# Kernel tuning notes

Hardware: AMD Instinct MI355X
Metric: run time of the kernel (lower is better)

Reference implementation:

```python
import jax, jax.numpy as jnp
import numpy as np
from jax import lax

N_GROUPS, TOP_K, CALIB_SCALE = 4, 3, 2.0


def setup_inputs() -> dict:
    key = jax.random.key(0)
    ks = jax.random.split(key, 32)
    d = {}
    d['x'] = jax.random.normal(ks[0], (64, 64, 8192), jnp.float32)
    d['conv_weight'] = jax.random.normal(ks[1], (64, 64, 3), jnp.float32) * 0.05
    d['bias'] = jax.random.normal(ks[2], (64,), jnp.float32) * 0.05
    d['grads'] = jax.random.normal(ks[3], (12288,), jnp.float32) * 0.01
    d['q_ema'] = jax.random.normal(ks[4], (4416,), jnp.float32) * 0.1
    d['ctrl_w'] = jax.random.normal(ks[5], (64, 192), jnp.float32) * 0.07
    d['ctrl_b'] = jnp.zeros((64,), jnp.float32)
    d['gp_w'] = jax.random.normal(ks[6], (64, 65), jnp.float32) * 0.1
    d['gp_b'] = jnp.zeros((64,), jnp.float32)
    d['gt_w'] = jax.random.normal(ks[7], (64, 64), jnp.float32) * 0.1
    d['gt_b'] = jnp.zeros((64,), jnp.float32)
    d['ln_g'] = jnp.ones((64,), jnp.float32)
    d['ln_b'] = jnp.zeros((64,), jnp.float32)
    d['ccin_w'] = jax.random.normal(ks[8], (64, 64), jnp.float32) * 0.05
    d['ccin_b'] = jnp.zeros((64,), jnp.float32)
    d['ck_w'] = jax.random.normal(ks[9], (3, 64), jnp.float32) * 0.05
    d['ck_b'] = jnp.zeros((3,), jnp.float32)
    d['cb_w'] = jax.random.normal(ks[10], (1, 64), jnp.float32) * 0.05
    d['cb_b'] = jnp.zeros((1,), jnp.float32)
    d['cf_w'] = jax.random.normal(ks[11], (1, 64), jnp.float32) * 0.05
    d['cf_b'] = jnp.zeros((1,), jnp.float32)
    d['tau_w'] = jax.random.normal(ks[12], (1, 64), jnp.float32) * 0.1
    d['tau_b'] = jnp.zeros((1,), jnp.float32)
    W = jax.random.normal(ks[13], (4, 1104, 32), jnp.float32)
    d['mem_W'] = W / jnp.linalg.norm(W, axis=1, keepdims=True)  # column-normalized codebook
    d['temp_logit'] = jnp.zeros((4,), jnp.float32)
    return d


def reference(x, conv_weight, bias, grads, q_ema, ctrl_w, ctrl_b, gp_w, gp_b,
              gt_w, gt_b, ln_g, ln_b, ccin_w, ccin_b, ck_w, ck_b, cb_w, cb_b,
              cf_w, cf_b, tau_w, tau_b, mem_W, temp_logit):
    C_out, C_in, K = conv_weight.shape
    cpg = C_out // N_GROUPS
    cin_tot, k_tot = C_out * C_in, C_out * K
    shift = 0.0  # shift_magnitude

    # --- controller: grads -> calibration query q ---
    g = grads.reshape(C_out, C_in * K)
    h = jax.nn.silu(g @ ctrl_w.T + ctrl_b)
    gn = jnp.linalg.norm(g, axis=-1, keepdims=True)
    z = jax.nn.sigmoid(jnp.concatenate([h, gn], -1) @ gp_w.T + gp_b)
    h_t = jax.nn.silu(h @ gt_w.T + gt_b)
    hm = (1.0 - z) * h + z * h_t
    mu = hm.mean(-1, keepdims=True)
    var = ((hm - mu) ** 2).mean(-1, keepdims=True)
    h = ln_g * (hm - mu) / jnp.sqrt(var + 1e-5) + ln_b

    w_cin = jnp.tanh(h @ ccin_w.T + ccin_b) * CALIB_SCALE   # [C_out, C_in]
    w_k = jnp.tanh(h @ ck_w.T + ck_b) * CALIB_SCALE         # [C_out, K]
    b_r = jnp.tanh(h @ cb_w.T + cb_b)[:, 0] * CALIB_SCALE   # [C_out]
    f_r = jnp.tanh(h @ cf_w.T + cf_b)[:, 0] * CALIB_SCALE   # [C_out]
    tau = jax.nn.sigmoid(h @ tau_w.T + tau_b).mean() * 0.5 + 0.5

    q = jnp.concatenate([w_cin.reshape(-1), w_k.reshape(-1), b_r, f_r])
    q = 0.7 * q + 0.3 * lax.stop_gradient(q_ema)

    # --- channel-grouped codebook retrieval (trigger path) ---
    qd = lax.stop_gradient(q)
    q_groups = jnp.concatenate([
        qd[:cin_tot].reshape(N_GROUPS, cpg * C_in),
        qd[cin_tot:cin_tot + k_tot].reshape(N_GROUPS, cpg * K),
        qd[cin_tot + k_tot:cin_tot + k_tot + C_out].reshape(N_GROUPS, cpg),
        qd[cin_tot + k_tot + C_out:].reshape(N_GROUPS, cpg)], axis=1)  # [G, gq]
    temp = (jax.nn.sigmoid(temp_logit) * 0.6 + 0.2) / (1.0 + shift)     # [G]
    att = jnp.einsum('gd,gdm->gm', q_groups, mem_W)
    att = jax.nn.softmax(att / (temp[:, None] + 1e-8), axis=1)
    v, idx = lax.top_k(att, TOP_K)                                      # [G, k]
    gath = jnp.take_along_axis(mem_W, idx[:, None, :], axis=2)          # [G, gq, k]
    retrieved = (gath * v[:, None, :]).sum(-1)                          # [G, gq]

    s0, s1, s2 = cpg * C_in, cpg * (C_in + K), cpg * (C_in + K + 1)
    retrieved_global = jnp.concatenate([
        retrieved[:, :s0].reshape(-1),
        retrieved[:, s0:s1].reshape(-1),
        retrieved[:, s1:s2].reshape(-1),
        retrieved[:, s2:].reshape(-1)])
    q = tau * q + (1.0 - tau) * lax.stop_gradient(retrieved_global)

    # --- split q and modulate conv ---
    w_cin = q[:cin_tot].reshape(C_out, C_in)
    w_k = q[cin_tot:cin_tot + k_tot].reshape(C_out, K)
    b_c = q[cin_tot + k_tot:cin_tot + k_tot + C_out]
    f_c = q[cin_tot + k_tot + C_out:]

    w = conv_weight * (1.0 + w_cin)[:, :, None] * (1.0 + w_k)[:, None, :]
    pad = ((K - 1) * 1 + 1) // 2  # receptive_field // 2 (dilation=1)
    out = lax.conv_general_dilated(x, w, window_strides=(1,),
                                   padding=[(pad, pad)], rhs_dilation=(1,),
                                   dimension_numbers=('NCH', 'OIH', 'NCH'))
    out = out + (bias * (1.0 + b_c))[None, :, None]
    out = out * (1.0 + f_c)[None, :, None]
    return out
```

## Files before the change

kernel.cpp:

```cpp
#include <hip/hip_runtime.h>
#include <math.h>

typedef __attribute__((ext_vector_type(8))) short bf16x8;
typedef __attribute__((ext_vector_type(4))) float f32x4;
typedef unsigned long long ull;

__device__ __forceinline__ float sigmoidf_(float x) { return 1.f / (1.f + expf(-x)); }

__device__ __forceinline__ unsigned short f2bf(float f) {
  unsigned int u = __float_as_uint(f);
  u += 0x7fffu + ((u >> 16) & 1u);
  return (unsigned short)(u >> 16);
}

#define WS_BEFF  0
#define WS_SEFF  64
#define WS_WFRAG 128

__global__ __launch_bounds__(1024) void kCtl(
    const float* __restrict__ grads, const float* __restrict__ ctrl_w, const float* __restrict__ ctrl_b,
    const float* __restrict__ gp_w, const float* __restrict__ gp_b,
    const float* __restrict__ gt_w, const float* __restrict__ gt_b,
    const float* __restrict__ ln_g, const float* __restrict__ ln_b,
    const float* __restrict__ ccin_w, const float* __restrict__ ccin_b,
    const float* __restrict__ ck_w, const float* __restrict__ ck_b,
    const float* __restrict__ cb_w, const float* __restrict__ cb_b,
    const float* __restrict__ cf_w, const float* __restrict__ cf_b,
    const float* __restrict__ tau_w, const float* __restrict__ tau_b,
    const float* __restrict__ q_ema, const float* __restrict__ mem_W,
    const float* __restrict__ temp_logit,
    const float* __restrict__ conv_weight, const float* __restrict__ bias,
    float* __restrict__ ws) {
  __shared__ float rawA[8514];
  __shared__ float sh_h[64 * 65];
  __shared__ float gnp[64 * 17];
  __shared__ float taup[64];
  __shared__ float sh_qg[4416];
  __shared__ float part[16][32];
  __shared__ float sv[3];
  __shared__ int sidx[3];
  __shared__ float qc1[16][64];
  __shared__ float qk1[16][3];
  __shared__ float sh_tau;
  const int tid = threadIdx.x;
  const int g = blockIdx.x;
  const int j = tid & 63;
  const int wv = tid >> 6;
  const int i0 = wv * 4;
  const int i0u = __builtin_amdgcn_readfirstlane(i0);

  float acc[4] = {0.f, 0.f, 0.f, 0.f};
  for (int hh = 0; hh < 2; ++hh) {
    const int d0 = hh * 96;
    for (int t = tid; t < 6144; t += 1024) {
      int jj = t / 96, dl = t - jj * 96;
      rawA[dl * 66 + jj] = ctrl_w[jj * 192 + d0 + dl];
    }
    __syncthreads();
    const float* g0 = grads + i0u * 192 + d0;
#pragma unroll 8
    for (int dl = 0; dl < 96; ++dl) {
      float wvv = rawA[dl * 66 + j];
      acc[0] += wvv * g0[dl];
      acc[1] += wvv * g0[192 + dl];
      acc[2] += wvv * g0[384 + dl];
      acc[3] += wvv * g0[576 + dl];
    }
    __syncthreads();
  }
  {
    float cb_ = ctrl_b[j];
#pragma unroll
    for (int ii = 0; ii < 4; ++ii) {
      float s = acc[ii] + cb_;
      sh_h[(i0 + ii) * 65 + j] = s * sigmoidf_(s);
    }
  }
  {
    int gi = tid >> 4, seg = tid & 15;
    const float* gr = grads + gi * 192 + seg * 12;
    float ss = 0.f;
#pragma unroll
    for (int m = 0; m < 12; ++m) { float v = gr[m]; ss += v * v; }
    gnp[gi * 17 + seg] = ss;
  }
  __syncthreads();
  if (tid < 64) {
    float s = 0.f;
#pragma unroll
    for (int seg = 0; seg < 16; ++seg) s += gnp[tid * 17 + seg];
    gnp[tid * 17 + 16] = sqrtf(s);
  }
  for (int t = tid; t < 4096; t += 1024) rawA[(t & 63) * 66 + (t >> 6)] = gt_w[t];
  for (int t = tid; t < 4160; t += 1024) {
    int jj = t / 65, dd = t - jj * 65;
    rawA[4224 + dd * 66 + jj] = gp_w[t];
  }
  __syncthreads();

  float hm[4];
  {
    float zacc[4] = {0.f, 0.f, 0.f, 0.f}, tacc[4] = {0.f, 0.f, 0.f, 0.f};
#pragma unroll 4
    for (int d = 0; d < 64; ++d) {
      float gtv = rawA[d * 66 + j];
      float gpv = rawA[4224 + d * 66 + j];
#pragma unroll
      for (int ii = 0; ii < 4; ++ii) {
        float hv = sh_h[(i0 + ii) * 65 + d];
        tacc[ii] += hv * gtv;
        zacc[ii] += hv * gpv;
      }
    }
    float gplast = rawA[4224 + 64 * 66 + j];
    float zb = gp_b[j], tb = gt_b[j];
#pragma unroll
    for (int ii = 0; ii < 4; ++ii) {
      float gn_ = gnp[(i0 + ii) * 17 + 16];
      float zs = zacc[ii] + gn_ * gplast + zb;
      float ts = tacc[ii] + tb;
      float z = sigmoidf_(zs);
      float ht = ts * sigmoidf_(ts);
      hm[ii] = (1.f - z) * sh_h[(i0 + ii) * 65 + j] + z * ht;
    }
  }
  __syncthreads();
#pragma unroll
  for (int ii = 0; ii < 4; ++ii) sh_h[(i0 + ii) * 65 + j] = hm[ii];
  __syncthreads();

  {
    float lg = ln_g[j], lb = ln_b[j];
#pragma unroll
    for (int ii = 0; ii < 4; ++ii) {
      float x = sh_h[(i0 + ii) * 65 + j];
      float s = x;
#pragma unroll
      for (int off = 32; off; off >>= 1) s += __shfl_xor(s, off);
      float mu = s * (1.f / 64.f);
      float dv = x - mu;
      float v2 = dv * dv;
#pragma unroll
      for (int off = 32; off; off >>= 1) v2 += __shfl_xor(v2, off);
      float invs = 1.f / sqrtf(v2 * (1.f / 64.f) + 1e-5f);
      sh_h[(i0 + ii) * 65 + j] = lg * dv * invs + lb;
    }
  }
  for (int t = tid; t < 4096; t += 1024) rawA[(t & 63) * 66 + (t >> 6)] = ccin_w[t];
  if (tid < 384) {
    int c = tid >> 6, d = tid & 63;
    float v = (c < 3) ? ck_w[c * 64 + d] : (c == 3) ? cb_w[d] : (c == 4) ? cf_w[d] : tau_w[d];
    rawA[4224 + c * 64 + d] = v;
  }
  __syncthreads();

  {
    float cb_ = ccin_b[j];
    float s4[4] = {0.f, 0.f, 0.f, 0.f};
#pragma unroll 4
    for (int d = 0; d < 64; ++d) {
      float cv = rawA[d * 66 + j];
#pragma unroll
      for (int ii = 0; ii < 4; ++ii) s4[ii] += sh_h[(i0 + ii) * 65 + d] * cv;
    }
#pragma unroll
    for (int ii = 0; ii < 4; ++ii) {
      int i = i0 + ii;
      float val = 2.f * tanhf(s4[ii] + cb_);
      sh_qg[(i >> 4) * 1104 + (i & 15) * 64 + j] = 0.7f * val + 0.3f * q_ema[i * 64 + j];
    }
  }
  if (wv < 6) {
    int i = j;
    float s = 0.f;
    const float* er = rawA + 4224 + wv * 64;
#pragma unroll 4
    for (int d = 0; d < 64; ++d) s += sh_h[i * 65 + d] * er[d];
    if (wv < 3) {
      float val = 2.f * tanhf(s + ck_b[wv]);
      sh_qg[(i >> 4) * 1104 + 1024 + (i & 15) * 3 + wv] = 0.7f * val + 0.3f * q_ema[4096 + i * 3 + wv];
    } else if (wv == 3) {
      float val = 2.f * tanhf(s + cb_b[0]);
      sh_qg[(i >> 4) * 1104 + 1072 + (i & 15)] = 0.7f * val + 0.3f * q_ema[4288 + i];
    } else if (wv == 4) {
      float val = 2.f * tanhf(s + cf_b[0]);
      sh_qg[(i >> 4) * 1104 + 1088 + (i & 15)] = 0.7f * val + 0.3f * q_ema[4352 + i];
    } else {
      taup[i] = sigmoidf_(s + tau_b[0]);
    }
  }
  __syncthreads();
  if (tid < 64) {
    float t_ = taup[tid];
#pragma unroll
    for (int off = 32; off; off >>= 1) t_ += __shfl_xor(t_, off);
    if (tid == 0) sh_tau = (t_ * (1.f / 64.f)) * 0.5f + 0.5f;
  }
  __syncthreads();

  const float* mwg = mem_W + (size_t)g * 1104 * 32;
  {
    float4 a = {0.f, 0.f, 0.f, 0.f};
    const float* qg = sh_qg + g * 1104;
#pragma unroll
    for (int it = 0; it < 9; ++it) {
      int d = it * 128 + (tid >> 3);
      if (d < 1104) {
        float4 v4 = *(const float4*)(mwg + (size_t)d * 32 + (tid & 7) * 4);
        float qv = qg[d];
        a.x += qv * v4.x; a.y += qv * v4.y; a.z += qv * v4.z; a.w += qv * v4.w;
      }
    }
#pragma unroll
    for (int off = 8; off <= 32; off <<= 1) {
      a.x += __shfl_xor(a.x, off); a.y += __shfl_xor(a.y, off);
      a.z += __shfl_xor(a.z, off); a.w += __shfl_xor(a.w, off);
    }
    if ((tid & 63) < 8) *(float4*)&part[tid >> 6][(tid & 7) * 4] = a;
  }
  __syncthreads();

  if (tid < 32) {
    int m = tid;
    float att = 0.f;
#pragma unroll
    for (int w = 0; w < 16; ++w) att += part[w][m];
    float temp = 0.6f * sigmoidf_(temp_logit[g]) + 0.2f;
    att /= (temp + 1e-8f);
    float mx = att;
#pragma unroll
    for (int off = 16; off; off >>= 1) mx = fmaxf(mx, __shfl_xor(mx, off, 32));
    float e = expf(att - mx);
    float s = e;
#pragma unroll
    for (int off = 16; off; off >>= 1) s += __shfl_xor(s, off, 32);
    float p = e / s;
    for (int t = 0; t < 3; ++t) {
      float bp = p; int bm = m;
#pragma unroll
      for (int off = 16; off; off >>= 1) {
        float op = __shfl_xor(bp, off, 32);
        int om = __shfl_xor(bm, off, 32);
        if (op > bp || (op == bp && om < bm)) { bp = op; bm = om; }
      }
      if (m == 0) { sv[t] = bp; sidx[t] = bm; }
      if (m == bm) p = -1.f;
    }
  }
  __syncthreads();

  {
    const float tau = sh_tau;
    const float v0 = sv[0], v1 = sv[1], v2 = sv[2];
    const int x0 = sidx[0], x1 = sidx[1], x2 = sidx[2];
    const float* qg = sh_qg + g * 1104;
    int cl = wv;
    int co = 16 * g + cl;
    int lane = j;
    {
      int d = cl * 64 + lane;
      float r = v0 * mwg[(size_t)d * 32 + x0] + v1 * mwg[(size_t)d * 32 + x1] + v2 * mwg[(size_t)d * 32 + x2];
      qc1[cl][lane] = 1.f + tau * qg[d] + (1.f - tau) * r;
    }
    if (lane < 3) {
      int d = 1024 + cl * 3 + lane;
      float r = v0 * mwg[(size_t)d * 32 + x0] + v1 * mwg[(size_t)d * 32 + x1] + v2 * mwg[(size_t)d * 32 + x2];
      qk1[cl][lane] = 1.f + tau * qg[d] + (1.f - tau) * r;
    }
    if (lane == 3) {
      int d = 1072 + cl;
      float r = v0 * mwg[(size_t)d * 32 + x0] + v1 * mwg[(size_t)d * 32 + x1] + v2 * mwg[(size_t)d * 32 + x2];
      float qb = tau * qg[d] + (1.f - tau) * r;
      ws[WS_BEFF + co] = bias[co] * (1.f + qb);
    }
    if (lane == 4) {
      int d = 1088 + cl;
      float r = v0 * mwg[(size_t)d * 32 + x0] + v1 * mwg[(size_t)d * 32 + x1] + v2 * mwg[(size_t)d * 32 + x2];
      ws[WS_SEFF + co] = 1.f + tau * qg[d] + (1.f - tau) * r;
    }
  }
  __syncthreads();

  unsigned short* wfrag = (unsigned short*)(ws + WS_WFRAG);
  for (int idx = tid; idx < 3072; idx += 1024) {
    int cl = idx / 192, rem = idx - cl * 192;
    int kk = rem >> 6, ci = rem & 63;
    int co = 16 * g + cl;
    float val = conv_weight[(co * 64 + ci) * 3 + kk] * qc1[cl][ci] * qk1[cl][kk];
    int e = kk * 64 + ci;
    int s = e >> 5, hi = (e >> 3) & 3, jj = e & 7;
    wfrag[s * 2048 + g * 512 + (16 * hi + cl) * 8 + jj] = f2bf(val);
  }
}

__global__ __launch_bounds__(256, 5) void k3_v7(
    const float* __restrict__ x, const unsigned short* __restrict__ wfrag,
    const float* __restrict__ beff, const float* __restrict__ seff,
    float* __restrict__ out) {
  __shared__ unsigned short xs[130 * 64];
  const int tid = threadIdx.x;
  const int w = tid >> 6, l = tid & 63;
  const int g = l >> 4, c16 = l & 15;
  const int n = blockIdx.y;
  const int l0 = blockIdx.x * 128;

  bf16x8 wf[6];
#pragma unroll
  for (int s = 0; s < 6; ++s)
    wf[s] = *(const bf16x8*)(wfrag + s * 2048 + w * 512 + l * 8);

  {
    const int cp = 8 * w + (l >> 3);
    const float* r0 = x + ((size_t)(n * 64 + 2 * cp)) * 8192 + l0;
    const float* r1 = r0 + 8192;
    char* xb = (char*)xs;
#pragma unroll
    for (int t = 0; t < 4; ++t) {
      int p0 = 4 * ((l & 7) + 8 * t);
      float4 va = *(const float4*)(r0 + p0);
      float4 vb = *(const float4*)(r1 + p0);
      float av[4] = {va.x, va.y, va.z, va.w};
      float bv[4] = {vb.x, vb.y, vb.z, vb.w};
#pragma unroll
      for (int i = 0; i < 4; ++i) {
        int p = p0 + i + 1;
        unsigned u = (unsigned)f2bf(av[i]) | ((unsigned)f2bf(bv[i]) << 16);
        *(unsigned*)(xb + p * 128 + ((4 * cp) ^ ((p & 7) << 4))) = u;
      }
    }
    if ((l & 7) == 0) {
      float a0 = 0.f, b0 = 0.f, a1 = 0.f, b1 = 0.f;
      if (l0 > 0) {
        float4 va = *(const float4*)(r0 - 4);
        float4 vb = *(const float4*)(r1 - 4);
        a0 = va.w; b0 = vb.w;
      }
      if (l0 + 128 < 8192) {
        float4 va = *(const float4*)(r0 + 128);
        float4 vb = *(const float4*)(r1 + 128);
        a1 = va.x; b1 = vb.x;
      }
      unsigned u0 = (unsigned)f2bf(a0) | ((unsigned)f2bf(b0) << 16);
      unsigned u1 = (unsigned)f2bf(a1) | ((unsigned)f2bf(b1) << 16);
      *(unsigned*)(xb + 0 * 128 + (4 * cp)) = u0;
      *(unsigned*)(xb + 129 * 128 + ((4 * cp) ^ 16)) = u1;
    }
  }
  __syncthreads();

  f32x4 acc[8];
#pragma unroll
  for (int t = 0; t < 8; ++t) acc[t] = (f32x4){0.f, 0.f, 0.f, 0.f};

  const char* xbc = (const char*)xs;
#pragma unroll
  for (int s = 0; s < 6; ++s) {
    const int kk = s >> 1;
    const int C = 4 * (s & 1) + g;
#pragma unroll
    for (int nt = 0; nt < 8; ++nt) {
      const int p = 16 * nt + c16 + kk;
      bf16x8 A = *(const bf16x8*)(xbc + p * 128 + ((C ^ (p & 7)) << 4));
      acc[nt] = __builtin_amdgcn_mfma_f32_16x16x32_bf16(A, wf[s], acc[nt], 0, 0, 0);
    }
  }

  const int co = 16 * w + c16;
  const float be = beff[co], se = seff[co];
  float* orow = out + ((size_t)(n * 64 + co)) * 8192 + l0 + 4 * g;
#pragma unroll
  for (int nt = 0; nt < 8; ++nt) {
    float4 ov;
    ov.x = se * (acc[nt][0] + be);
    ov.y = se * (acc[nt][1] + be);
    ov.z = se * (acc[nt][2] + be);
    ov.w = se * (acc[nt][3] + be);
    *(float4*)(orow + nt * 16) = ov;
  }
}

extern "C" void kernel_launch(void* const* d_in, const int* in_sizes, int n_in,
                              void* d_out, int out_size, void* d_ws, size_t ws_size,
                              hipStream_t stream) {
  const float* x = (const float*)d_in[0];
  const float* conv_weight = (const float*)d_in[1];
  const float* bias = (const float*)d_in[2];
  const float* grads = (const float*)d_in[3];
  const float* q_ema = (const float*)d_in[4];
  const float* ctrl_w = (const float*)d_in[5];
  const float* ctrl_b = (const float*)d_in[6];
  const float* gp_w = (const float*)d_in[7];
  const float* gp_b = (const float*)d_in[8];
  const float* gt_w = (const float*)d_in[9];
  const float* gt_b = (const float*)d_in[10];
  const float* ln_g = (const float*)d_in[11];
  const float* ln_b = (const float*)d_in[12];
  const float* ccin_w = (const float*)d_in[13];
  const float* ccin_b = (const float*)d_in[14];
  const float* ck_w = (const float*)d_in[15];
  const float* ck_b = (const float*)d_in[16];
  const float* cb_w = (const float*)d_in[17];
  const float* cb_b = (const float*)d_in[18];
  const float* cf_w = (const float*)d_in[19];
  const float* cf_b = (const float*)d_in[20];
  const float* tau_w = (const float*)d_in[21];
  const float* tau_b = (const float*)d_in[22];
  const float* mem_W = (const float*)d_in[23];
  const float* temp_logit = (const float*)d_in[24];

  float* ws = (float*)d_ws;

  hipLaunchKernelGGL(kCtl, dim3(4), dim3(1024), 0, stream,
                     grads, ctrl_w, ctrl_b, gp_w, gp_b, gt_w, gt_b, ln_g, ln_b,
                     ccin_w, ccin_b, ck_w, ck_b, cb_w, cb_b, cf_w, cf_b,
                     tau_w, tau_b, q_ema, mem_W, temp_logit, conv_weight, bias, ws);
  hipLaunchKernelGGL(k3_v7, dim3(64, 64), dim3(256), 0, stream,
                     x, (const unsigned short*)(ws + WS_WFRAG), ws + WS_BEFF, ws + WS_SEFF,
                     (float*)d_out);
}
```

Baseline: 100.8 us.

## Make conv blocks persistent over four tiles with double-buffered LDS prefetch

Each block now processes four consecutive 128-wide tiles instead of one. Global loads for the next tile are issued before the MFMA work on the current tile and written to the second LDS buffer afterwards. This overlaps the memory traffic with compute and loads the weight fragments once per four tiles. In exchange it launches a quarter as many blocks, uses twice the LDS and holds more live registers, which lowers occupancy (launch bounds drop from 5 to 4).

```diff
diff --git a/kernel.cpp b/kernel.cpp
--- a/kernel.cpp
+++ b/kernel.cpp
@@ -7,10 +7,10 @@
 
 __device__ __forceinline__ float sigmoidf_(float x) { return 1.f / (1.f + expf(-x)); }
 
-__device__ __forceinline__ unsigned short f2bf(float f) {
+__device__ __forceinline__ unsigned f2bf(float f) {
   unsigned int u = __float_as_uint(f);
   u += 0x7fffu + ((u >> 16) & 1u);
-  return (unsigned short)(u >> 16);
+  return u >> 16;
 }
 
 #define WS_BEFF  0
@@ -289,94 +289,124 @@
     float val = conv_weight[(co * 64 + ci) * 3 + kk] * qc1[cl][ci] * qk1[cl][kk];
     int e = kk * 64 + ci;
     int s = e >> 5, hi = (e >> 3) & 3, jj = e & 7;
-    wfrag[s * 2048 + g * 512 + (16 * hi + cl) * 8 + jj] = f2bf(val);
+    wfrag[s * 2048 + g * 512 + (16 * hi + cl) * 8 + jj] = (unsigned short)f2bf(val);
   }
 }
 
-__global__ __launch_bounds__(256, 5) void k3_v7(
+#define TC 4
+__global__ __launch_bounds__(256, 4) void k3_p(
     const float* __restrict__ x, const unsigned short* __restrict__ wfrag,
     const float* __restrict__ beff, const float* __restrict__ seff,
     float* __restrict__ out) {
-  __shared__ unsigned short xs[130 * 64];
+  __shared__ unsigned short xs[2][130 * 64];
   const int tid = threadIdx.x;
   const int w = tid >> 6, l = tid & 63;
   const int g = l >> 4, c16 = l & 15;
   const int n = blockIdx.y;
-  const int l0 = blockIdx.x * 128;
+  const int base = blockIdx.x * (TC * 128);
 
   bf16x8 wf[6];
 #pragma unroll
   for (int s = 0; s < 6; ++s)
     wf[s] = *(const bf16x8*)(wfrag + s * 2048 + w * 512 + l * 8);
 
-  {
-    const int cp = 8 * w + (l >> 3);
-    const float* r0 = x + ((size_t)(n * 64 + 2 * cp)) * 8192 + l0;
-    const float* r1 = r0 + 8192;
-    char* xb = (char*)xs;
-#pragma unroll
-    for (int t = 0; t < 4; ++t) {
-      int p0 = 4 * ((l & 7) + 8 * t);
-      float4 va = *(const float4*)(r0 + p0);
-      float4 vb = *(const float4*)(r1 + p0);
-      float av[4] = {va.x, va.y, va.z, va.w};
-      float bv[4] = {vb.x, vb.y, vb.z, vb.w};
-#pragma unroll
-      for (int i = 0; i < 4; ++i) {
-        int p = p0 + i + 1;
-        unsigned u = (unsigned)f2bf(av[i]) | ((unsigned)f2bf(bv[i]) << 16);
-        *(unsigned*)(xb + p * 128 + ((4 * cp) ^ ((p & 7) << 4))) = u;
-      }
-    }
-    if ((l & 7) == 0) {
-      float a0 = 0.f, b0 = 0.f, a1 = 0.f, b1 = 0.f;
-      if (l0 > 0) {
-        float4 va = *(const float4*)(r0 - 4);
-        float4 vb = *(const float4*)(r1 - 4);
-        a0 = va.w; b0 = vb.w;
-      }
-      if (l0 + 128 < 8192) {
-        float4 va = *(const float4*)(r0 + 128);
-        float4 vb = *(const float4*)(r1 + 128);
-        a1 = va.x; b1 = vb.x;
-      }
-      unsigned u0 = (unsigned)f2bf(a0) | ((unsigned)f2bf(b0) << 16);
-      unsigned u1 = (unsigned)f2bf(a1) | ((unsigned)f2bf(b1) << 16);
-      *(unsigned*)(xb + 0 * 128 + (4 * cp)) = u0;
-      *(unsigned*)(xb + 129 * 128 + ((4 * cp) ^ 16)) = u1;
-    }
-  }
-  __syncthreads();
-
-  f32x4 acc[8];
-#pragma unroll
-  for (int t = 0; t < 8; ++t) acc[t] = (f32x4){0.f, 0.f, 0.f, 0.f};
-
-  const char* xbc = (const char*)xs;
-#pragma unroll
-  for (int s = 0; s < 6; ++s) {
-    const int kk = s >> 1;
-    const int C = 4 * (s & 1) + g;
-#pragma unroll
-    for (int nt = 0; nt < 8; ++nt) {
-      const int p = 16 * nt + c16 + kk;
-      bf16x8 A = *(const bf16x8*)(xbc + p * 128 + ((C ^ (p & 7)) << 4));
-      acc[nt] = __builtin_amdgcn_mfma_f32_16x16x32_bf16(A, wf[s], acc[nt], 0, 0, 0);
-    }
-  }
-
+  const int cp = 8 * w + (l >> 3);
+  const float* r0 = x + ((size_t)(n * 64 + 2 * cp)) * 8192;
+  const float* r1 = r0 + 8192;
+  const bool hlane = ((l & 7) == 0);
   const int co = 16 * w + c16;
   const float be = beff[co], se = seff[co];
-  float* orow = out + ((size_t)(n * 64 + co)) * 8192 + l0 + 4 * g;
-#pragma unroll
-  for (int nt = 0; nt < 8; ++nt) {
-    float4 ov;
-    ov.x = se * (acc[nt][0] + be);
-    ov.y = se * (acc[nt][1] + be);
-    ov.z = se * (acc[nt][2] + be);
-    ov.w = se * (acc[nt][3] + be);
-    *(float4*)(orow + nt * 16) = ov;
-  }
+
+  float4 va0, va1, va2, va3, vb0, vb1, vb2, vb3;
+  float ha0, hb0, ha1, hb1;
+
+#define ISSUE_LOADS(L0)                                                     \
+  {                                                                         \
+    const int pb = (L0) + 4 * (l & 7);                                      \
+    va0 = *(const float4*)(r0 + pb);       vb0 = *(const float4*)(r1 + pb); \
+    va1 = *(const float4*)(r0 + pb + 32);  vb1 = *(const float4*)(r1 + pb + 32); \
+    va2 = *(const float4*)(r0 + pb + 64);  vb2 = *(const float4*)(r1 + pb + 64); \
+    va3 = *(const float4*)(r0 + pb + 96);  vb3 = *(const float4*)(r1 + pb + 96); \
+    ha0 = hb0 = ha1 = hb1 = 0.f;                                            \
+    if (hlane) {                                                            \
+      if ((L0) > 0) { ha0 = r0[(L0) - 1]; hb0 = r1[(L0) - 1]; }             \
+      if ((L0) + 128 < 8192) { ha1 = r0[(L0) + 128]; hb1 = r1[(L0) + 128]; } \
+    }                                                                       \
+  }
+
+#define WRITE_LDS(BUF)                                                      \
+  {                                                                         \
+    char* xb = (char*)xs[BUF];                                              \
+    float av[16] = {va0.x, va0.y, va0.z, va0.w, va1.x, va1.y, va1.z, va1.w, \
+                    va2.x, va2.y, va2.z, va2.w, va3.x, va3.y, va3.z, va3.w}; \
+    float bv[16] = {vb0.x, vb0.y, vb0.z, vb0.w, vb1.x, vb1.y, vb1.z, vb1.w, \
+                    vb2.x, vb2.y, vb2.z, vb2.w, vb3.x, vb3.y, vb3.z, vb3.w}; \
+    _Pragma("unroll")                                                       \
+    for (int t = 0; t < 4; ++t) {                                           \
+      int p0 = 4 * ((l & 7) + 8 * t);                                       \
+      _Pragma("unroll")                                                     \
+      for (int i = 0; i < 4; ++i) {                                         \
+        int p = p0 + i + 1;                                                 \
+        unsigned u = f2bf(av[4 * t + i]) | (f2bf(bv[4 * t + i]) << 16);     \
+        *(unsigned*)(xb + p * 128 + ((4 * cp) ^ ((p & 7) << 4))) = u;       \
+      }                                                                     \
+    }                                                                       \
+    if (hlane) {                                                            \
+      *(unsigned*)(xb + 4 * cp) = f2bf(ha0) | (f2bf(hb0) << 16);            \
+      *(unsigned*)(xb + 129 * 128 + ((4 * cp) ^ 16)) = f2bf(ha1) | (f2bf(hb1) << 16); \
+    }                                                                       \
+  }
+
+  ISSUE_LOADS(base);
+  WRITE_LDS(0);
+  __builtin_amdgcn_sched_barrier(0);
+  asm volatile("s_waitcnt lgkmcnt(0)" ::: "memory");
+  __builtin_amdgcn_sched_barrier(0);
+  __builtin_amdgcn_s_barrier();
+  __builtin_amdgcn_sched_barrier(0);
+
+#pragma unroll
+  for (int t = 0; t < TC; ++t) {
+    const int l0 = base + t * 128;
+    if (t + 1 < TC) ISSUE_LOADS(l0 + 128);
+
+    f32x4 acc[8];
+#pragma unroll
+    for (int q = 0; q < 8; ++q) acc[q] = (f32x4){0.f, 0.f, 0.f, 0.f};
+    const char* xbc = (const char*)xs[t & 1];
+#pragma unroll
+    for (int s = 0; s < 6; ++s) {
+      const int kk = s >> 1;
+      const int C = 4 * (s & 1) + g;
+#pragma unroll
+      for (int nt = 0; nt < 8; ++nt) {
+        const int p = 16 * nt + c16 + kk;
+        bf16x8 A = *(const bf16x8*)(xbc + p * 128 + ((C ^ (p & 7)) << 4));
+        acc[nt] = __builtin_amdgcn_mfma_f32_16x16x32_bf16(A, wf[s], acc[nt], 0, 0, 0);
+      }
+    }
+    float* orow = out + ((size_t)(n * 64 + co)) * 8192 + l0 + 4 * g;
+#pragma unroll
+    for (int nt = 0; nt < 8; ++nt) {
+      float4 ov;
+      ov.x = se * (acc[nt][0] + be);
+      ov.y = se * (acc[nt][1] + be);
+      ov.z = se * (acc[nt][2] + be);
+      ov.w = se * (acc[nt][3] + be);
+      *(float4*)(orow + nt * 16) = ov;
+    }
+
+    if (t + 1 < TC) {
+      WRITE_LDS((t + 1) & 1);
+      __builtin_amdgcn_sched_barrier(0);
+      asm volatile("s_waitcnt lgkmcnt(0)" ::: "memory");
+      __builtin_amdgcn_sched_barrier(0);
+      __builtin_amdgcn_s_barrier();
+      __builtin_amdgcn_sched_barrier(0);
+    }
+  }
+#undef ISSUE_LOADS
+#undef WRITE_LDS
 }
 
 extern "C" void kernel_launch(void* const* d_in, const int* in_sizes, int n_in,
@@ -414,7 +444,7 @@
                      grads, ctrl_w, ctrl_b, gp_w, gp_b, gt_w, gt_b, ln_g, ln_b,
                      ccin_w, ccin_b, ck_w, ck_b, cb_w, cb_b, cf_w, cf_b,
                      tau_w, tau_b, q_ema, mem_W, temp_logit, conv_weight, bias, ws);
-  hipLaunchKernelGGL(k3_v7, dim3(64, 64), dim3(256), 0, stream,
+  hipLaunchKernelGGL(k3_p, dim3(16, 64), dim3(256), 0, stream,
                      x, (const unsigned short*)(ws + WS_WFRAG), ws + WS_BEFF, ws + WS_SEFF,
                      (float*)d_out);
 }
```

New measurement: 112.4 us. +11.5%, slower.

## Double-buffer x tiles via direct global-to-LDS loads and shift-based conv taps

Applied to the files above, without the earlier changes.

Replaces the main conv kernel with one where each block covers 256 positions in four 64-wide chunks. The chunks are staged through two LDS buffers using global_load_lds, with manual vmcnt waits so loads overlap MFMA work. Instead of reading shifted windows per tap, the kernel computes all three tap products on unshifted tiles and combines them with cross-lane shuffles, a carried value and halo corrections. The fp32-to-bf16 conversion moves from staging to the LDS read path. The hand-tuned wait counts and the carry logic are fragile, and the kernel now does more conversion work per MFMA and runs fewer blocks.

```diff
diff --git a/kernel.cpp b/kernel.cpp
--- a/kernel.cpp
+++ b/kernel.cpp
@@ -7,10 +7,13 @@
 
 __device__ __forceinline__ float sigmoidf_(float x) { return 1.f / (1.f + expf(-x)); }
 
-__device__ __forceinline__ unsigned short f2bf(float f) {
+__device__ __forceinline__ unsigned f2bf(float f) {
   unsigned int u = __float_as_uint(f);
   u += 0x7fffu + ((u >> 16) & 1u);
-  return (unsigned short)(u >> 16);
+  return u >> 16;
+}
+__device__ __forceinline__ float bf2f(unsigned short u) {
+  return __uint_as_float(((unsigned int)u) << 16);
 }
 
 #define WS_BEFF  0
@@ -289,94 +292,143 @@
     float val = conv_weight[(co * 64 + ci) * 3 + kk] * qc1[cl][ci] * qk1[cl][kk];
     int e = kk * 64 + ci;
     int s = e >> 5, hi = (e >> 3) & 3, jj = e & 7;
-    wfrag[s * 2048 + g * 512 + (16 * hi + cl) * 8 + jj] = f2bf(val);
+    wfrag[s * 2048 + g * 512 + (16 * hi + cl) * 8 + jj] = (unsigned short)f2bf(val);
   }
 }
 
-__global__ __launch_bounds__(256, 5) void k3_v7(
+__global__ __launch_bounds__(256, 4) void k3_g(
     const float* __restrict__ x, const unsigned short* __restrict__ wfrag,
     const float* __restrict__ beff, const float* __restrict__ seff,
     float* __restrict__ out) {
-  __shared__ unsigned short xs[130 * 64];
+  __shared__ unsigned xsb[2][64 * 65];
+  __shared__ float lhal[64], rhal[64];
   const int tid = threadIdx.x;
   const int w = tid >> 6, l = tid & 63;
   const int g = l >> 4, c16 = l & 15;
   const int n = blockIdx.y;
-  const int l0 = blockIdx.x * 128;
+  const int base = blockIdx.x * 256;
 
   bf16x8 wf[6];
 #pragma unroll
   for (int s = 0; s < 6; ++s)
     wf[s] = *(const bf16x8*)(wfrag + s * 2048 + w * 512 + l * 8);
 
-  {
-    const int cp = 8 * w + (l >> 3);
-    const float* r0 = x + ((size_t)(n * 64 + 2 * cp)) * 8192 + l0;
-    const float* r1 = r0 + 8192;
-    char* xb = (char*)xs;
-#pragma unroll
-    for (int t = 0; t < 4; ++t) {
-      int p0 = 4 * ((l & 7) + 8 * t);
-      float4 va = *(const float4*)(r0 + p0);
-      float4 vb = *(const float4*)(r1 + p0);
-      float av[4] = {va.x, va.y, va.z, va.w};
-      float bv[4] = {vb.x, vb.y, vb.z, vb.w};
-#pragma unroll
-      for (int i = 0; i < 4; ++i) {
-        int p = p0 + i + 1;
-        unsigned u = (unsigned)f2bf(av[i]) | ((unsigned)f2bf(bv[i]) << 16);
-        *(unsigned*)(xb + p * 128 + ((4 * cp) ^ ((p & 7) << 4))) = u;
-      }
-    }
-    if ((l & 7) == 0) {
-      float a0 = 0.f, b0 = 0.f, a1 = 0.f, b1 = 0.f;
-      if (l0 > 0) {
-        float4 va = *(const float4*)(r0 - 4);
-        float4 vb = *(const float4*)(r1 - 4);
-        a0 = va.w; b0 = vb.w;
-      }
-      if (l0 + 128 < 8192) {
-        float4 va = *(const float4*)(r0 + 128);
-        float4 vb = *(const float4*)(r1 + 128);
-        a1 = va.x; b1 = vb.x;
-      }
-      unsigned u0 = (unsigned)f2bf(a0) | ((unsigned)f2bf(b0) << 16);
-      unsigned u1 = (unsigned)f2bf(a1) | ((unsigned)f2bf(b1) << 16);
-      *(unsigned*)(xb + 0 * 128 + (4 * cp)) = u0;
-      *(unsigned*)(xb + 129 * 128 + ((4 * cp) ^ 16)) = u1;
-    }
-  }
-  __syncthreads();
-
-  f32x4 acc[8];
-#pragma unroll
-  for (int t = 0; t < 8; ++t) acc[t] = (f32x4){0.f, 0.f, 0.f, 0.f};
-
-  const char* xbc = (const char*)xs;
-#pragma unroll
-  for (int s = 0; s < 6; ++s) {
-    const int kk = s >> 1;
-    const int C = 4 * (s & 1) + g;
-#pragma unroll
-    for (int nt = 0; nt < 8; ++nt) {
-      const int p = 16 * nt + c16 + kk;
-      bf16x8 A = *(const bf16x8*)(xbc + p * 128 + ((C ^ (p & 7)) << 4));
-      acc[nt] = __builtin_amdgcn_mfma_f32_16x16x32_bf16(A, wf[s], acc[nt], 0, 0, 0);
-    }
-  }
+  if (tid < 64) {
+    const float* rowp = x + ((size_t)(n * 64 + tid)) * 8192;
+    lhal[tid] = (base > 0) ? rowp[base - 1] : 0.f;
+    rhal[tid] = (base + 256 < 8192) ? rowp[base + 256] : 0.f;
+  }
+
+#define STAGE(BUF, L0)                                                        \
+  {                                                                           \
+    __builtin_amdgcn_sched_barrier(0);                                        \
+    _Pragma("unroll") for (int i_ = 0; i_ < 16; ++i_) {                       \
+      int ci_ = 16 * w + i_;                                                  \
+      __builtin_amdgcn_global_load_lds(                                       \
+          (const __attribute__((address_space(1))) void*)(                    \
+              x + ((size_t)(n * 64 + ci_)) * 8192 + (L0) + l),                \
+          (__attribute__((address_space(3))) void*)(&xsb[BUF][ci_ * 65]),     \
+          4, 0, 0);                                                           \
+    }                                                                         \
+    __builtin_amdgcn_sched_barrier(0);                                        \
+  }
+
+  STAGE(0, base)
+  STAGE(1, base + 64)
 
   const int co = 16 * w + c16;
   const float be = beff[co], se = seff[co];
-  float* orow = out + ((size_t)(n * 64 + co)) * 8192 + l0 + 4 * g;
-#pragma unroll
-  for (int nt = 0; nt < 8; ++nt) {
+  float* orow = out + ((size_t)(n * 64 + co)) * 8192 + 4 * g;
+
+  float carry0 = 0.f, s2s = 0.f;
+  f32x4 pend;
+  float* pendAddr = orow;
+
+#define BARRIER1(VMC)                                                         \
+  asm volatile("s_waitcnt vmcnt(" #VMC ") lgkmcnt(0)" ::: "memory");          \
+  __builtin_amdgcn_sched_barrier(0);                                          \
+  __builtin_amdgcn_s_barrier();                                               \
+  __builtin_amdgcn_sched_barrier(0);
+
+#define COMPUTE(T, BUF)                                                       \
+  {                                                                           \
+    const float* xf = (const float*)xsb[BUF];                                 \
+    const int l0_ = base + (T) * 64;                                          \
+    _Pragma("unroll") for (int nt = 0; nt < 4; ++nt) {                        \
+      union { bf16x8 v; unsigned u[4]; } A0, A1;                              \
+      _Pragma("unroll") for (int k = 0; k < 4; ++k) {                         \
+        int pb0 = (8 * g + 2 * k) * 65 + 16 * nt + c16;                       \
+        A0.u[k] = f2bf(xf[pb0]) | (f2bf(xf[pb0 + 65]) << 16);                 \
+        int pb1 = (32 + 8 * g + 2 * k) * 65 + 16 * nt + c16;                  \
+        A1.u[k] = f2bf(xf[pb1]) | (f2bf(xf[pb1 + 65]) << 16);                 \
+      }                                                                       \
+      f32x4 o = (f32x4){0.f, 0.f, 0.f, 0.f};                                  \
+      f32x4 y0 = o, y2 = o;                                                   \
+      o  = __builtin_amdgcn_mfma_f32_16x16x32_bf16(A0.v, wf[2], o, 0, 0, 0);  \
+      o  = __builtin_amdgcn_mfma_f32_16x16x32_bf16(A1.v, wf[3], o, 0, 0, 0);  \
+      y0 = __builtin_amdgcn_mfma_f32_16x16x32_bf16(A0.v, wf[0], y0, 0, 0, 0); \
+      y0 = __builtin_amdgcn_mfma_f32_16x16x32_bf16(A1.v, wf[1], y0, 0, 0, 0); \
+      y2 = __builtin_amdgcn_mfma_f32_16x16x32_bf16(A0.v, wf[4], y2, 0, 0, 0); \
+      y2 = __builtin_amdgcn_mfma_f32_16x16x32_bf16(A1.v, wf[5], y2, 0, 0, 0); \
+      float sh_ = __shfl(y0[3], (l - 16) & 63);                               \
+      o[0] += (g == 0) ? carry0 : sh_;                                        \
+      o[1] += y0[0]; o[2] += y0[1]; o[3] += y0[2];                            \
+      carry0 = sh_;                                                           \
+      float b0_ = __shfl(y2[0], (l + 16) & 63);                               \
+      o[0] += y2[1]; o[1] += y2[2]; o[2] += y2[3];                            \
+      o[3] += (g < 3) ? b0_ : 0.f;                                            \
+      if ((T) > 0 || nt > 0) {                                                \
+        pend[3] += (g == 3) ? b0_ : 0.f;                                      \
+        float4 ov_;                                                           \
+        ov_.x = se * (pend[0] + be); ov_.y = se * (pend[1] + be);             \
+        ov_.z = se * (pend[2] + be); ov_.w = se * (pend[3] + be);             \
+        *(float4*)pendAddr = ov_;                                             \
+      }                                                                       \
+      pend = o;                                                               \
+      pendAddr = orow + l0_ + nt * 16;                                        \
+    }                                                                         \
+  }
+
+  BARRIER1(16)
+  {
+    float s0 = 0.f, s2 = 0.f;
+#pragma unroll
+    for (int h = 0; h < 2; ++h)
+#pragma unroll
+      for (int j = 0; j < 8; ++j) {
+        int ci = 32 * h + 8 * g + j;
+        s0 += bf2f((unsigned short)wf[h][j]) * lhal[ci];
+        s2 += bf2f((unsigned short)wf[4 + h][j]) * rhal[ci];
+      }
+    s0 += __shfl_xor(s0, 16); s0 += __shfl_xor(s0, 32);
+    s2 += __shfl_xor(s2, 16); s2 += __shfl_xor(s2, 32);
+    carry0 = s0; s2s = s2;
+  }
+  COMPUTE(0, 0)
+  __builtin_amdgcn_s_barrier();
+  STAGE(0, base + 128)
+
+  BARRIER1(19)
+  COMPUTE(1, 1)
+  __builtin_amdgcn_s_barrier();
+  STAGE(1, base + 192)
+
+  BARRIER1(20)
+  COMPUTE(2, 0)
+
+  BARRIER1(4)
+  COMPUTE(3, 1)
+
+  pend[3] += (g == 3) ? s2s : 0.f;
+  {
     float4 ov;
-    ov.x = se * (acc[nt][0] + be);
-    ov.y = se * (acc[nt][1] + be);
-    ov.z = se * (acc[nt][2] + be);
-    ov.w = se * (acc[nt][3] + be);
-    *(float4*)(orow + nt * 16) = ov;
-  }
+    ov.x = se * (pend[0] + be); ov.y = se * (pend[1] + be);
+    ov.z = se * (pend[2] + be); ov.w = se * (pend[3] + be);
+    *(float4*)pendAddr = ov;
+  }
+#undef STAGE
+#undef BARRIER1
+#undef COMPUTE
 }
 
 extern "C" void kernel_launch(void* const* d_in, const int* in_sizes, int n_in,
@@ -414,7 +466,7 @@
                      grads, ctrl_w, ctrl_b, gp_w, gp_b, gt_w, gt_b, ln_g, ln_b,
                      ccin_w, ccin_b, ck_w, ck_b, cb_w, cb_b, cf_w, cf_b,
                      tau_w, tau_b, q_ema, mem_W, temp_logit, conv_weight, bias, ws);
-  hipLaunchKernelGGL(k3_v7, dim3(64, 64), dim3(256), 0, stream,
+  hipLaunchKernelGGL(k3_g, dim3(32, 64), dim3(256), 0, stream,
                      x, (const unsigned short*)(ws + WS_WFRAG), ws + WS_BEFF, ws + WS_SEFF,
                      (float*)d_out);
 }
```

Measured after the change: 166.0 us. 64.6% more time.
